# Optimization experiments

Measured on AMD Instinct MI355X. Metric: run time of the kernel, lower is better.

## Reference

```python
import jax, jax.numpy as jnp
import numpy as np

DIM = 16
BOND = 4
RANK = 512
N = 50000
E = 400000
F_IN = 16
EDGE_VARIABLE = 2


def setup_inputs() -> dict:
    key = jax.random.key(0)
    ks = iter(jax.random.split(key, 48))
    g = lambda shape, s=0.1: jax.random.normal(next(ks), shape, jnp.float32) * s
    inp = {
        "x": jax.random.normal(next(ks), (N, F_IN), jnp.float32),
        "node_type": jax.random.randint(next(ks), (N,), 0, 3),
        "edge_index": jax.random.randint(next(ks), (2, E), 0, N),
        "edge_attr": jax.random.uniform(next(ks), (E, BOND), dtype=jnp.float32),
        # lin0
        "W_lin0": g((F_IN, DIM)), "b_lin0": jnp.zeros((DIM,), jnp.float32),
        # NNConv: root weight + edge-conditioned weight MLP (4 -> 32 -> dim*dim)
        "W_root": g((DIM, DIM)), "b_conv": jnp.zeros((DIM,), jnp.float32),
        "W_e1": g((BOND, 32)), "b_e1": jnp.zeros((32,), jnp.float32),
        "W_e2": g((32, DIM * DIM)), "b_e2": jnp.zeros((DIM * DIM,), jnp.float32),
        # GRU (torch gate order r,z,n), weights stored torch-style [3*dim, dim]
        "W_ih": g((3 * DIM, DIM)), "b_ih": jnp.zeros((3 * DIM,), jnp.float32),
        "W_hh": g((3 * DIM, DIM)), "b_hh": jnp.zeros((3 * DIM,), jnp.float32),
        # projections
        "W_lin1": g((DIM, BOND)), "b_lin1": jnp.zeros((BOND,), jnp.float32),
        "W_up": g((BOND, DIM)), "b_up": jnp.zeros((DIM,), jnp.float32),
        "W_down": g((DIM, BOND)), "b_down": jnp.zeros((BOND,), jnp.float32),
        # FGNet low-rank factor modules (rank 512)
        "U_B": g((DIM, RANK)), "V_B": g((RANK, DIM)),
        "U_C": g((DIM, RANK)), "V_C": g((RANK, DIM)),
        "U_A": g((BOND, RANK)), "V_A": g((RANK, BOND)),
        # fusion weights
        "w_node": g((1, DIM)), "W_lin": g((DIM, DIM)), "b_lin": jnp.zeros((DIM,), jnp.float32),
        "w_edge": g((1, BOND)), "W_line": g((BOND, BOND)), "b_line": jnp.zeros((BOND,), jnp.float32),
    }
    return inp


def _forward(x, edge_attr, W_lin0, b_lin0, W_root, b_conv, W_e1, b_e1, W_e2, b_e2,
             W_ih, b_ih, W_hh, b_hh, W_lin1, b_lin1, W_up, b_up, W_down, b_down,
             U_B, V_B, U_C, V_C, U_A, V_A, w_node, W_lin, b_lin, w_edge, W_line, b_line,
             node_type, edge_index):
    src, dst = edge_index[0], edge_index[1]

    def nnconv(out):
        # per-edge weight matrices from edge features (edge-conditioned conv)
        he = jax.nn.relu(edge_attr @ W_e1 + b_e1)
        We = (he @ W_e2 + b_e2).reshape(E, DIM, DIM)          # [E, dim, dim]
        m = jnp.einsum('ed,edk->ek', out[src], We)             # gather-multiply
        agg = jax.ops.segment_sum(m, dst, num_segments=N)      # scatter-add
        deg = jax.ops.segment_sum(jnp.ones((E,), out.dtype), dst, num_segments=N)
        agg = agg / jnp.clip(deg, 1.0)[:, None]                # mean aggregation
        return out @ W_root + b_conv + agg

    def gru(inp, h):
        gi = inp @ W_ih.T + b_ih
        gh = h @ W_hh.T + b_hh
        i_r, i_z, i_n = jnp.split(gi, 3, axis=-1)
        h_r, h_z, h_n = jnp.split(gh, 3, axis=-1)
        r = jax.nn.sigmoid(i_r + h_r)
        z = jax.nn.sigmoid(i_z + h_z)
        n = jnp.tanh(i_n + r * h_n)
        return (1.0 - z) * n + z * h

    out = jax.nn.relu(x @ W_lin0 + b_lin0)                     # [N, dim]
    h = out
    for _ in range(3):
        m = jax.nn.relu(nnconv(out))
        h = gru(m, h)
        out = h

    out_edges = jax.nn.relu(out @ W_lin1 + b_lin1)             # [N, bond]

    # one outer message-passing round (k in range(1))
    ev_mask = (node_type == EDGE_VARIABLE)[:, None]
    out_edges_up = out_edges @ W_up + b_up                     # [N, dim]
    out_combine = jnp.where(ev_mask, out_edges_up, out)        # masked replace

    # factor-B message (low-rank FGNet) -> node-dim message + down-projected edge msg
    msg_B = jax.nn.relu((out_combine @ U_B) @ V_B)             # [N, dim]
    msg_to_edge_B = msg_B @ W_down + b_down                    # [N, bond]

    # factor-C message (low-rank FGNet)
    msg_C = jax.nn.relu((out_combine @ U_C) @ V_C)             # [N, dim]

    # factor-A / valence message on edge-type beliefs
    msg_to_edge_A = jax.nn.relu((out_edges @ U_A) @ V_A)       # [N, bond]

    all_msg = msg_B + msg_C                                    # sum over stacked msgs
    combine_edge_msg = msg_to_edge_A * msg_to_edge_B

    out = out + jax.nn.relu((w_node * all_msg) @ W_lin + b_lin)
    out_edges = out_edges + jax.nn.relu((w_edge * combine_edge_msg) @ W_line + b_line)

    return jax.nn.log_softmax(out_edges, axis=-1)              # [N, bond]


def reference(x, node_type, edge_index, edge_attr, W_lin0, b_lin0, W_root, b_conv,
              W_e1, b_e1, W_e2, b_e2, W_ih, b_ih, W_hh, b_hh, W_lin1, b_lin1,
              W_up, b_up, W_down, b_down, U_B, V_B, U_C, V_C, U_A, V_A,
              w_node, W_lin, b_lin, w_edge, W_line, b_line):
    return _forward(x, edge_attr, W_lin0, b_lin0, W_root, b_conv, W_e1, b_e1, W_e2, b_e2,
                    W_ih, b_ih, W_hh, b_hh, W_lin1, b_lin1, W_up, b_up, W_down, b_down,
                    U_B, V_B, U_C, V_C, U_A, V_A, w_node, W_lin, b_lin, w_edge, W_line, b_line,
                    node_type, edge_index)
```

## Files before the change

### kernel.cpp

```cpp
#include <hip/hip_runtime.h>
#include <hip/hip_bf16.h>
#include <math.h>

#define N_NODES 50000
#define N_EDGES 400000
#define DIM 16
#define BOND 4
#define NCHUNK 25000
#define EDGE_GRID 784
#define E_BLOCKS 1563
#define PRE_BASE (E_BLOCKS - 68)
#define SCAN_TILE 1024
#define SCAN_BLOCKS 49

typedef __attribute__((ext_vector_type(8))) short short8;
typedef __attribute__((ext_vector_type(4))) float f32x4;

__device__ __forceinline__ float bf16_to_f32(unsigned short v) {
  return __uint_as_float(((unsigned int)v) << 16);
}

__global__ __launch_bounds__(256) void setup_kernel(
    const float* __restrict__ x, const float* __restrict__ W_lin0,
    const float* __restrict__ b_lin0, const int* __restrict__ ei,
    const float* __restrict__ U_B, const float* __restrict__ V_B,
    const float* __restrict__ U_A, const float* __restrict__ V_A,
    float* __restrict__ out, int* __restrict__ degI, int* __restrict__ rank,
    float* __restrict__ M_B, float* __restrict__ M_A) {
  __shared__ float sW0[256];
  __shared__ float sb0[16];
  int t = threadIdx.x;
  sW0[t] = W_lin0[t];
  if (t < 16) sb0[t] = b_lin0[t];
  __syncthreads();

  int gid = blockIdx.x * 256 + t;

  if (gid < N_NODES) {
    float xr[16];
#pragma unroll
    for (int d = 0; d < 16; ++d) xr[d] = x[gid * 16 + d];
#pragma unroll
    for (int k = 0; k < 16; ++k) {
      float acc = sb0[k];
#pragma unroll
      for (int d = 0; d < 16; ++d) acc += xr[d] * sW0[d * 16 + k];
      out[gid * 16 + k] = fmaxf(acc, 0.f);
    }
  }

  if (gid < N_EDGES) {
    rank[gid] = atomicAdd(&degI[ei[N_EDGES + gid]], 1);
  }

  if (blockIdx.x >= PRE_BASE) {
    int w = (blockIdx.x - PRE_BASE) * 4 + (t >> 6);
    int lane = t & 63;
    float partial = 0.f;
    if (w < 256) {
      int i = w >> 4, j = w & 15;
#pragma unroll
      for (int r8 = 0; r8 < 8; ++r8) {
        int r = lane + 64 * r8;
        partial += U_B[i * 512 + r] * V_B[r * 16 + j];
      }
    } else if (w < 272) {
      int a = (w - 256) >> 2, b = (w - 256) & 3;
#pragma unroll
      for (int r8 = 0; r8 < 8; ++r8) {
        int r = lane + 64 * r8;
        partial += U_A[a * 512 + r] * V_A[r * 4 + b];
      }
    }
#pragma unroll
    for (int off = 32; off > 0; off >>= 1)
      partial += __shfl_down(partial, off);
    if (lane == 0) {
      if (w < 256) M_B[w] = partial;
      else if (w < 272) M_A[w - 256] = partial;
    }
  }
}

__global__ __launch_bounds__(256) void scan_kernel(
    const int* __restrict__ degI, int* ticket, int* st,
    int* __restrict__ row_off) {
  __shared__ int sdata[256];
  __shared__ int s_tile;
  __shared__ int s_base;
  int t = threadIdx.x;
  if (t == 0) s_tile = atomicAdd(ticket, 1);
  __syncthreads();
  int tile = s_tile;
  int n0 = tile * SCAN_TILE + t * 4;

  int d0 = (n0 + 0 < N_NODES) ? degI[n0 + 0] : 0;
  int d1 = (n0 + 1 < N_NODES) ? degI[n0 + 1] : 0;
  int d2 = (n0 + 2 < N_NODES) ? degI[n0 + 2] : 0;
  int d3 = (n0 + 3 < N_NODES) ? degI[n0 + 3] : 0;
  int tsum = d0 + d1 + d2 + d3;
  sdata[t] = tsum;
  __syncthreads();
  for (int off = 1; off < 256; off <<= 1) {
    int v = (t >= off) ? sdata[t - off] : 0;
    __syncthreads();
    sdata[t] += v;
    __syncthreads();
  }
  int excl = sdata[t] - tsum;
  int agg = sdata[255];

  if (t == 0) {
    if (tile == 0) {
      atomicExch(&st[0], (agg << 2) | 2);
      s_base = 0;
    } else {
      atomicExch(&st[tile], (agg << 2) | 1);
      int run = 0, idx = tile - 1;
      while (true) {
        int w = atomicAdd(&st[idx], 0);
        int stt = w & 3;
        if (stt == 2) { run += (w >> 2); break; }
        if (stt == 1) { run += (w >> 2); --idx; }
      }
      atomicExch(&st[tile], ((run + agg) << 2) | 2);
      s_base = run;
    }
  }
  __syncthreads();

  int pre = s_base + excl;
  if (n0 + 0 < N_NODES) row_off[n0 + 0] = pre;
  pre += d0;
  if (n0 + 1 < N_NODES) row_off[n0 + 1] = pre;
  pre += d1;
  if (n0 + 2 < N_NODES) row_off[n0 + 2] = pre;
  pre += d2;
  if (n0 + 3 < N_NODES) row_off[n0 + 3] = pre;
  if (tile == SCAN_BLOCKS - 1 && t == 0) row_off[N_NODES] = N_EDGES;
}

__global__ __launch_bounds__(256) void edge_msg_mfma_kernel(
    const int* __restrict__ ei, const float* __restrict__ ea,
    const float* __restrict__ We1, const float* __restrict__ be1,
    const float* __restrict__ We2, const float* __restrict__ be2,
    const float* __restrict__ out, const int* __restrict__ row_off,
    const int* __restrict__ rank, unsigned short* __restrict__ m_bufh) {
  __shared__ float sW1T[128];
  __shared__ float sbe1[32];
  int t = threadIdx.x;
  if (t < 128) sW1T[t] = We1[(t & 3) * 32 + 2 * ((t >> 2) & 15) + (t >> 6)];
  if (t < 32) sbe1[t] = be1[2 * (t & 15) + (t >> 4)];

  const int lane = t & 63;
  const int q = lane >> 4, n = lane & 15;
  const int p = q >> 1, dbase = (q & 1) * 8;

  short8 bfrag[17];
#pragma unroll
  for (int s = 0; s < 16; ++s) {
    int h = 2 * s + p;
    union { short8 v; __hip_bfloat162 b2[4]; } bf;
#pragma unroll
    for (int jj = 0; jj < 4; ++jj) {
      float2 w;
      w.x = We2[h * 256 + (dbase + 2 * jj) * 16 + n];
      w.y = We2[h * 256 + (dbase + 2 * jj + 1) * 16 + n];
      bf.b2[jj] = __float22bfloat162_rn(w);
    }
    bfrag[s] = bf.v;
  }
  {
    union { short8 v; __hip_bfloat162 b2[4]; } bf;
#pragma unroll
    for (int jj = 0; jj < 4; ++jj) {
      float2 w;
      if (q < 2) {
        w.x = be2[(dbase + 2 * jj) * 16 + n];
        w.y = be2[(dbase + 2 * jj + 1) * 16 + n];
      } else {
        w.x = 0.f; w.y = 0.f;
      }
      bf.b2[jj] = __float22bfloat162_rn(w);
    }
    bfrag[16] = bf.v;
  }
  __syncthreads();

  int wave = blockIdx.x * 4 + (t >> 6);
  const int nw = EDGE_GRID * 4;
  for (int c = wave; c < NCHUNK; c += nw) {
    int base = c * 16;
    int e = base + n;
    int4 dst4 = *(const int4*)(ei + N_EDGES + base + q * 4);
    int4 rk4 = *(const int4*)(rank + base + q * 4);
    int src = ei[e];
    float4 av = ((const float4*)ea)[e];
    int slx = row_off[dst4.x] + rk4.x;
    int sly = row_off[dst4.y] + rk4.y;
    int slz = row_off[dst4.z] + rk4.z;
    int slw = row_off[dst4.w] + rk4.w;
    const float4* op = (const float4*)(out + src * 16 + dbase);
    float4 o0 = op[0], o1 = op[1];
    float o[8] = {o0.x, o0.y, o0.z, o0.w, o1.x, o1.y, o1.z, o1.w};

    f32x4 acc = {0.f, 0.f, 0.f, 0.f};
#pragma unroll
    for (int s = 0; s < 16; ++s) {
      float4 wj = *(const float4*)&sW1T[(p * 16 + s) * 4];
      float he_s = fmaxf(sbe1[p * 16 + s] + av.x * wj.x + av.y * wj.y +
                             av.z * wj.z + av.w * wj.w,
                         0.f);
      union { short8 v; __hip_bfloat162 b2[4]; } af;
#pragma unroll
      for (int jj = 0; jj < 4; ++jj) {
        float2 pr;
        pr.x = he_s * o[2 * jj];
        pr.y = he_s * o[2 * jj + 1];
        af.b2[jj] = __float22bfloat162_rn(pr);
      }
      acc = __builtin_amdgcn_mfma_f32_16x16x32_bf16(af.v, bfrag[s], acc, 0, 0, 0);
    }
    {
      union { short8 v; __hip_bfloat162 b2[4]; } af;
#pragma unroll
      for (int jj = 0; jj < 4; ++jj) {
        float2 pr;
        if (q < 2) { pr.x = o[2 * jj]; pr.y = o[2 * jj + 1]; }
        else { pr.x = 0.f; pr.y = 0.f; }
        af.b2[jj] = __float22bfloat162_rn(pr);
      }
      acc = __builtin_amdgcn_mfma_f32_16x16x32_bf16(af.v, bfrag[16], acc, 0, 0, 0);
    }

    __hip_bfloat16 b0 = __float2bfloat16(acc[0]);
    __hip_bfloat16 b1 = __float2bfloat16(acc[1]);
    __hip_bfloat16 b2 = __float2bfloat16(acc[2]);
    __hip_bfloat16 b3 = __float2bfloat16(acc[3]);
    m_bufh[(size_t)slx * 16 + n] = *(unsigned short*)&b0;
    m_bufh[(size_t)sly * 16 + n] = *(unsigned short*)&b1;
    m_bufh[(size_t)slz * 16 + n] = *(unsigned short*)&b2;
    m_bufh[(size_t)slw * 16 + n] = *(unsigned short*)&b3;
  }
}

__global__ __launch_bounds__(256) void gather_gru_kernel(
    const int* __restrict__ row_off, const unsigned short* __restrict__ m_bufh,
    const float* __restrict__ Wroot, const float* __restrict__ bconv,
    const float* __restrict__ Wih, const float* __restrict__ bih,
    const float* __restrict__ Whh, const float* __restrict__ bhh,
    float* __restrict__ out, int do_final, const int* __restrict__ node_type,
    const float* __restrict__ Wlin1, const float* __restrict__ blin1,
    const float* __restrict__ Wup, const float* __restrict__ bup,
    const float* __restrict__ Wdown, const float* __restrict__ bdown,
    const float* __restrict__ M_B, const float* __restrict__ M_A,
    const float* __restrict__ wedge, const float* __restrict__ Wline,
    const float* __restrict__ bline, float* __restrict__ res) {
  __shared__ float sWr[256];
  __shared__ float sWihT[768];
  __shared__ float sWhhT[768];
  __shared__ float sb[112];
  int t = threadIdx.x;
  int kk = t >> 4, dd = t & 15;
  sWr[t] = Wroot[t];
#pragma unroll
  for (int g = 0; g < 3; ++g) {
    sWihT[g * 256 + dd * 16 + kk] = Wih[g * 256 + t];
    sWhhT[g * 256 + dd * 16 + kk] = Whh[g * 256 + t];
  }
  if (t < 16) sb[t] = bconv[t];
  else if (t < 64) sb[t] = bih[t - 16];
  else if (t < 112) sb[t] = bhh[t - 64];
  __syncthreads();

  int n = blockIdx.x * 16 + (t >> 4);
  int k = t & 15;
  int s0 = row_off[n], s1 = row_off[n + 1];

  float aggk = 0.f;
  for (int j = s0; j < s1; ++j) aggk += bf16_to_f32(m_bufh[(size_t)j * 16 + k]);
  float sc = 1.f / fmaxf((float)(s1 - s0), 1.f);

  float hk = out[n * 16 + k];

  float mk = sb[k] + aggk * sc;
#pragma unroll
  for (int d = 0; d < 16; ++d) mk += __shfl(hk, d, 16) * sWr[d * 16 + k];
  mk = fmaxf(mk, 0.f);

  float gir = sb[16 + k], giz = sb[32 + k], gin = sb[48 + k];
  float ghr = sb[64 + k], ghz = sb[80 + k], ghn = sb[96 + k];
#pragma unroll
  for (int d = 0; d < 16; ++d) {
    float md = __shfl(mk, d, 16);
    float hd = __shfl(hk, d, 16);
    gir += md * sWihT[d * 16 + k];
    giz += md * sWihT[256 + d * 16 + k];
    gin += md * sWihT[512 + d * 16 + k];
    ghr += hd * sWhhT[d * 16 + k];
    ghz += hd * sWhhT[256 + d * 16 + k];
    ghn += hd * sWhhT[512 + d * 16 + k];
  }
  float r = 1.f / (1.f + __expf(-(gir + ghr)));
  float z = 1.f / (1.f + __expf(-(giz + ghz)));
  float xn = gin + r * ghn;
  float ng = 1.f - 2.f / (__expf(2.f * xn) + 1.f);
  float hnew = (1.f - z) * ng + z * hk;

  if (!do_final) {
    out[n * 16 + k] = hnew;
    return;
  }

  float p0 = hnew * Wlin1[k * 4 + 0];
  float p1 = hnew * Wlin1[k * 4 + 1];
  float p2 = hnew * Wlin1[k * 4 + 2];
  float p3 = hnew * Wlin1[k * 4 + 3];
#pragma unroll
  for (int msk = 1; msk < 16; msk <<= 1) {
    p0 += __shfl_xor(p0, msk, 16);
    p1 += __shfl_xor(p1, msk, 16);
    p2 += __shfl_xor(p2, msk, 16);
    p3 += __shfl_xor(p3, msk, 16);
  }
  float oe0 = fmaxf(p0 + blin1[0], 0.f);
  float oe1 = fmaxf(p1 + blin1[1], 0.f);
  float oe2 = fmaxf(p2 + blin1[2], 0.f);
  float oe3 = fmaxf(p3 + blin1[3], 0.f);

  bool ev = (node_type[n] == 2);
  float ock = ev ? (bup[k] + oe0 * Wup[k] + oe1 * Wup[16 + k] +
                    oe2 * Wup[32 + k] + oe3 * Wup[48 + k])
                 : hnew;

  float msgBk = 0.f;
#pragma unroll
  for (int d = 0; d < 16; ++d) msgBk += __shfl(ock, d, 16) * M_B[d * 16 + k];
  msgBk = fmaxf(msgBk, 0.f);

  float q0 = msgBk * Wdown[k * 4 + 0];
  float q1 = msgBk * Wdown[k * 4 + 1];
  float q2 = msgBk * Wdown[k * 4 + 2];
  float q3 = msgBk * Wdown[k * 4 + 3];
#pragma unroll
  for (int msk = 1; msk < 16; msk <<= 1) {
    q0 += __shfl_xor(q0, msk, 16);
    q1 += __shfl_xor(q1, msk, 16);
    q2 += __shfl_xor(q2, msk, 16);
    q3 += __shfl_xor(q3, msk, 16);
  }
  float mtb0 = q0 + bdown[0], mtb1 = q1 + bdown[1];
  float mtb2 = q2 + bdown[2], mtb3 = q3 + bdown[3];

  float mta0 = fmaxf(oe0 * M_A[0] + oe1 * M_A[4] + oe2 * M_A[8] + oe3 * M_A[12], 0.f);
  float mta1 = fmaxf(oe0 * M_A[1] + oe1 * M_A[5] + oe2 * M_A[9] + oe3 * M_A[13], 0.f);
  float mta2 = fmaxf(oe0 * M_A[2] + oe1 * M_A[6] + oe2 * M_A[10] + oe3 * M_A[14], 0.f);
  float mta3 = fmaxf(oe0 * M_A[3] + oe1 * M_A[7] + oe2 * M_A[11] + oe3 * M_A[15], 0.f);

  float c0 = wedge[0] * (mta0 * mtb0);
  float c1 = wedge[1] * (mta1 * mtb1);
  float c2 = wedge[2] * (mta2 * mtb2);
  float c3 = wedge[3] * (mta3 * mtb3);

  float f0 = oe0 + fmaxf(bline[0] + c0 * Wline[0] + c1 * Wline[4] +
                         c2 * Wline[8] + c3 * Wline[12], 0.f);
  float f1 = oe1 + fmaxf(bline[1] + c0 * Wline[1] + c1 * Wline[5] +
                         c2 * Wline[9] + c3 * Wline[13], 0.f);
  float f2 = oe2 + fmaxf(bline[2] + c0 * Wline[2] + c1 * Wline[6] +
                         c2 * Wline[10] + c3 * Wline[14], 0.f);
  float f3 = oe3 + fmaxf(bline[3] + c0 * Wline[3] + c1 * Wline[7] +
                         c2 * Wline[11] + c3 * Wline[15], 0.f);

  float mx = fmaxf(fmaxf(f0, f1), fmaxf(f2, f3));
  float se = __expf(f0 - mx) + __expf(f1 - mx) + __expf(f2 - mx) +
             __expf(f3 - mx);
  float lse = mx + __logf(se);
  if (k < 4) {
    float v = (k == 0) ? f0 : (k == 1) ? f1 : (k == 2) ? f2 : f3;
    res[n * 4 + k] = v - lse;
  }
}

extern "C" void kernel_launch(void* const* d_in, const int* in_sizes, int n_in,
                              void* d_out, int out_size, void* d_ws,
                              size_t ws_size, hipStream_t stream) {
  const float* x       = (const float*)d_in[0];
  const int* node_type = (const int*)d_in[1];
  const int* ei        = (const int*)d_in[2];
  const float* ea      = (const float*)d_in[3];
  const float* W_lin0  = (const float*)d_in[4];
  const float* b_lin0  = (const float*)d_in[5];
  const float* W_root  = (const float*)d_in[6];
  const float* b_conv  = (const float*)d_in[7];
  const float* W_e1    = (const float*)d_in[8];
  const float* b_e1    = (const float*)d_in[9];
  const float* W_e2    = (const float*)d_in[10];
  const float* b_e2    = (const float*)d_in[11];
  const float* W_ih    = (const float*)d_in[12];
  const float* b_ih    = (const float*)d_in[13];
  const float* W_hh    = (const float*)d_in[14];
  const float* b_hh    = (const float*)d_in[15];
  const float* W_lin1  = (const float*)d_in[16];
  const float* b_lin1  = (const float*)d_in[17];
  const float* W_up    = (const float*)d_in[18];
  const float* b_up    = (const float*)d_in[19];
  const float* W_down  = (const float*)d_in[20];
  const float* b_down  = (const float*)d_in[21];
  const float* U_B     = (const float*)d_in[22];
  const float* V_B     = (const float*)d_in[23];
  const float* U_A     = (const float*)d_in[26];
  const float* V_A     = (const float*)d_in[27];
  const float* w_edge  = (const float*)d_in[31];
  const float* W_line  = (const float*)d_in[32];
  const float* b_line  = (const float*)d_in[33];

  float* ws    = (float*)d_ws;
  float* out   = ws;
  unsigned short* m_bufh = (unsigned short*)(out + N_NODES * 16);
  float* M_B   = (float*)(m_bufh + (size_t)N_EDGES * 16);
  float* M_A   = M_B + 256;
  int* degI    = (int*)(M_A + 16);
  int* ticket  = degI + N_NODES;
  int* st      = ticket + 1;
  int* row_off = st + 63;
  int* rank    = row_off + N_NODES + 1;

  hipMemsetAsync(degI, 0, (N_NODES + 64) * sizeof(int), stream);

  setup_kernel<<<E_BLOCKS, 256, 0, stream>>>(x, W_lin0, b_lin0, ei, U_B, V_B,
                                             U_A, V_A, out, degI, rank, M_B,
                                             M_A);
  scan_kernel<<<SCAN_BLOCKS, 256, 0, stream>>>(degI, ticket, st, row_off);

  for (int it = 0; it < 3; ++it) {
    edge_msg_mfma_kernel<<<EDGE_GRID, 256, 0, stream>>>(
        ei, ea, W_e1, b_e1, W_e2, b_e2, out, row_off, rank, m_bufh);
    gather_gru_kernel<<<N_NODES / 16, 256, 0, stream>>>(
        row_off, m_bufh, W_root, b_conv, W_ih, b_ih, W_hh, b_hh, out,
        (it == 2) ? 1 : 0, node_type, W_lin1, b_lin1, W_up, b_up, W_down,
        b_down, M_B, M_A, w_edge, W_line, b_line, (float*)d_out);
  }
}
```

Measured before the change: 360.2 us.

## Precompute CSR slots once and software-pipeline edge loads in message kernel

Adds a slot kernel that computes each edge's CSR destination slot once, replacing the per-iteration row_off[dst]+rank indirect lookups in the edge message kernel. The edge loop now prefetches edge indices, attributes and slots two chunks ahead and the source node features one chunk ahead, to hide global load latency behind the MFMA work. The gather loop is unrolled by four to expose more independent loads. The costs are an extra launch, a slot buffer in the workspace, and higher register pressure from the prefetch state.

After: 324.7 us. 1.11x faster.

```diff
diff --git a/kernel.cpp b/kernel.cpp
--- a/kernel.cpp
+++ b/kernel.cpp
@@ -140,12 +140,19 @@
   if (tile == SCAN_BLOCKS - 1 && t == 0) row_off[N_NODES] = N_EDGES;
 }
 
+__global__ __launch_bounds__(256) void slot_kernel(
+    const int* __restrict__ ei, const int* __restrict__ row_off,
+    const int* __restrict__ rank, int* __restrict__ slot) {
+  int e = blockIdx.x * 256 + threadIdx.x;
+  if (e < N_EDGES) slot[e] = row_off[ei[N_EDGES + e]] + rank[e];
+}
+
 __global__ __launch_bounds__(256) void edge_msg_mfma_kernel(
     const int* __restrict__ ei, const float* __restrict__ ea,
     const float* __restrict__ We1, const float* __restrict__ be1,
     const float* __restrict__ We2, const float* __restrict__ be2,
-    const float* __restrict__ out, const int* __restrict__ row_off,
-    const int* __restrict__ rank, unsigned short* __restrict__ m_bufh) {
+    const float* __restrict__ out, const int* __restrict__ slot,
+    unsigned short* __restrict__ m_bufh) {
   __shared__ float sW1T[128];
   __shared__ float sbe1[32];
   int t = threadIdx.x;
@@ -187,29 +194,57 @@
   }
   __syncthreads();
 
-  int wave = blockIdx.x * 4 + (t >> 6);
+  const int wave = blockIdx.x * 4 + (t >> 6);
   const int nw = EDGE_GRID * 4;
+
+  int srcP = 0, srcQ = 0;
+  float4 avP = {0.f, 0.f, 0.f, 0.f}, avQ = {0.f, 0.f, 0.f, 0.f};
+  int4 slP = {0, 0, 0, 0}, slQ = {0, 0, 0, 0};
+  float4 oP0 = {0.f, 0.f, 0.f, 0.f}, oP1 = {0.f, 0.f, 0.f, 0.f};
+
+  if (wave < NCHUNK) {
+    int e = wave * 16 + n;
+    srcP = ei[e];
+    avP = ((const float4*)ea)[e];
+    slP = *(const int4*)(slot + wave * 16 + q * 4);
+  }
+  if (wave + nw < NCHUNK) {
+    int e = (wave + nw) * 16 + n;
+    srcQ = ei[e];
+    avQ = ((const float4*)ea)[e];
+    slQ = *(const int4*)(slot + (wave + nw) * 16 + q * 4);
+  }
+  if (wave < NCHUNK) {
+    const float4* op = (const float4*)(out + srcP * 16 + dbase);
+    oP0 = op[0];
+    oP1 = op[1];
+  }
+
   for (int c = wave; c < NCHUNK; c += nw) {
-    int base = c * 16;
-    int e = base + n;
-    int4 dst4 = *(const int4*)(ei + N_EDGES + base + q * 4);
-    int4 rk4 = *(const int4*)(rank + base + q * 4);
-    int src = ei[e];
-    float4 av = ((const float4*)ea)[e];
-    int slx = row_off[dst4.x] + rk4.x;
-    int sly = row_off[dst4.y] + rk4.y;
-    int slz = row_off[dst4.z] + rk4.z;
-    int slw = row_off[dst4.w] + rk4.w;
-    const float4* op = (const float4*)(out + src * 16 + dbase);
-    float4 o0 = op[0], o1 = op[1];
-    float o[8] = {o0.x, o0.y, o0.z, o0.w, o1.x, o1.y, o1.z, o1.w};
-
+    int srcN = 0;
+    float4 avN = {0.f, 0.f, 0.f, 0.f};
+    int4 slN = {0, 0, 0, 0};
+    int cn2 = c + 2 * nw;
+    if (cn2 < NCHUNK) {
+      int e = cn2 * 16 + n;
+      srcN = ei[e];
+      avN = ((const float4*)ea)[e];
+      slN = *(const int4*)(slot + cn2 * 16 + q * 4);
+    }
+    float4 oQ0 = {0.f, 0.f, 0.f, 0.f}, oQ1 = {0.f, 0.f, 0.f, 0.f};
+    if (c + nw < NCHUNK) {
+      const float4* op = (const float4*)(out + srcQ * 16 + dbase);
+      oQ0 = op[0];
+      oQ1 = op[1];
+    }
+
+    float o[8] = {oP0.x, oP0.y, oP0.z, oP0.w, oP1.x, oP1.y, oP1.z, oP1.w};
     f32x4 acc = {0.f, 0.f, 0.f, 0.f};
 #pragma unroll
     for (int s = 0; s < 16; ++s) {
       float4 wj = *(const float4*)&sW1T[(p * 16 + s) * 4];
-      float he_s = fmaxf(sbe1[p * 16 + s] + av.x * wj.x + av.y * wj.y +
-                             av.z * wj.z + av.w * wj.w,
+      float he_s = fmaxf(sbe1[p * 16 + s] + avP.x * wj.x + avP.y * wj.y +
+                             avP.z * wj.z + avP.w * wj.w,
                          0.f);
       union { short8 v; __hip_bfloat162 b2[4]; } af;
 #pragma unroll
@@ -237,10 +272,13 @@
     __hip_bfloat16 b1 = __float2bfloat16(acc[1]);
     __hip_bfloat16 b2 = __float2bfloat16(acc[2]);
     __hip_bfloat16 b3 = __float2bfloat16(acc[3]);
-    m_bufh[(size_t)slx * 16 + n] = *(unsigned short*)&b0;
-    m_bufh[(size_t)sly * 16 + n] = *(unsigned short*)&b1;
-    m_bufh[(size_t)slz * 16 + n] = *(unsigned short*)&b2;
-    m_bufh[(size_t)slw * 16 + n] = *(unsigned short*)&b3;
+    m_bufh[(size_t)slP.x * 16 + n] = *(unsigned short*)&b0;
+    m_bufh[(size_t)slP.y * 16 + n] = *(unsigned short*)&b1;
+    m_bufh[(size_t)slP.z * 16 + n] = *(unsigned short*)&b2;
+    m_bufh[(size_t)slP.w * 16 + n] = *(unsigned short*)&b3;
+
+    avP = avQ; slP = slQ; oP0 = oQ0; oP1 = oQ1;
+    srcQ = srcN; avQ = avN; slQ = slN;
   }
 }
 
@@ -278,7 +316,15 @@
   int s0 = row_off[n], s1 = row_off[n + 1];
 
   float aggk = 0.f;
-  for (int j = s0; j < s1; ++j) aggk += bf16_to_f32(m_bufh[(size_t)j * 16 + k]);
+  int j = s0;
+  for (; j + 3 < s1; j += 4) {
+    float a0 = bf16_to_f32(m_bufh[(size_t)(j + 0) * 16 + k]);
+    float a1 = bf16_to_f32(m_bufh[(size_t)(j + 1) * 16 + k]);
+    float a2 = bf16_to_f32(m_bufh[(size_t)(j + 2) * 16 + k]);
+    float a3 = bf16_to_f32(m_bufh[(size_t)(j + 3) * 16 + k]);
+    aggk += (a0 + a1) + (a2 + a3);
+  }
+  for (; j < s1; ++j) aggk += bf16_to_f32(m_bufh[(size_t)j * 16 + k]);
   float sc = 1.f / fmaxf((float)(s1 - s0), 1.f);
 
   float hk = out[n * 16 + k];
@@ -424,6 +470,7 @@
   int* st      = ticket + 1;
   int* row_off = st + 63;
   int* rank    = row_off + N_NODES + 1;
+  int* slot    = rank + N_EDGES;
 
   hipMemsetAsync(degI, 0, (N_NODES + 64) * sizeof(int), stream);
 
@@ -431,10 +478,11 @@
                                              U_A, V_A, out, degI, rank, M_B,
                                              M_A);
   scan_kernel<<<SCAN_BLOCKS, 256, 0, stream>>>(degI, ticket, st, row_off);
+  slot_kernel<<<E_BLOCKS, 256, 0, stream>>>(ei, row_off, rank, slot);
 
   for (int it = 0; it < 3; ++it) {
     edge_msg_mfma_kernel<<<EDGE_GRID, 256, 0, stream>>>(
-        ei, ea, W_e1, b_e1, W_e2, b_e2, out, row_off, rank, m_bufh);
+        ei, ea, W_e1, b_e1, W_e2, b_e2, out, slot, m_bufh);
     gather_gru_kernel<<<N_NODES / 16, 256, 0, stream>>>(
         row_off, m_bufh, W_root, b_conv, W_ih, b_ih, W_hh, b_hh, out,
         (it == 2) ? 1 : 0, node_type, W_lin1, b_lin1, W_up, b_up, W_down,
```
